# Performance work log

Hardware: AMD Instinct MI355X
Metric: run time of the kernel (lower is better)

The kernel has to match this reference:

```python
import jax, jax.numpy as jnp
import numpy as np

B, T, V, E, H = 32, 40, 8000, 50, 2048


def setup_inputs() -> dict:
    key = jax.random.key(0)
    ks = jax.random.split(key, 13)
    s = 0.02  # small init scale for stability
    return {
        "features": jax.random.normal(ks[0], (B, H), dtype=jnp.float32),
        "captions": jax.random.randint(ks[1], (B, T), 0, V),
        "emb": jax.random.normal(ks[2], (V, E), dtype=jnp.float32) * s,
        "lstm_Wih": jax.random.normal(ks[3], (4 * H, E), dtype=jnp.float32) * s,
        "lstm_bih": jax.random.normal(ks[4], (4 * H,), dtype=jnp.float32) * s,
        "lstm_Whh": jax.random.normal(ks[5], (4 * H, H), dtype=jnp.float32) * s,
        "lstm_bhh": jax.random.normal(ks[6], (4 * H,), dtype=jnp.float32) * s,
        "gru_Wih": jax.random.normal(ks[7], (3 * H, H), dtype=jnp.float32) * s,
        "gru_bih": jax.random.normal(ks[8], (3 * H,), dtype=jnp.float32) * s,
        "gru_Whh": jax.random.normal(ks[9], (3 * H, H), dtype=jnp.float32) * s,
        "gru_bhh": jax.random.normal(ks[10], (3 * H,), dtype=jnp.float32) * s,
        "lin_W": jax.random.normal(ks[11], (V, H), dtype=jnp.float32) * s,
        "lin_b": jax.random.normal(ks[12], (V,), dtype=jnp.float32) * s,
    }


def reference(features, captions, emb, lstm_Wih, lstm_bih, lstm_Whh, lstm_bhh,
              gru_Wih, gru_bih, gru_Whh, gru_bhh, lin_W, lin_b):
    # Dropout layers act as identity in eval mode.
    embeddings = emb[captions]                 # [B, T, E]
    xs = jnp.swapaxes(embeddings[:, :-1], 0, 1)  # [T-1, B, E]

    def step(carry, x):
        h_l, c_l, h_g = carry
        # torch LSTMCell
        gates = x @ lstm_Wih.T + lstm_bih + h_l @ lstm_Whh.T + lstm_bhh
        i, f, g, o = jnp.split(gates, 4, axis=-1)
        c = jax.nn.sigmoid(f) * c_l + jax.nn.sigmoid(i) * jnp.tanh(g)
        h = jax.nn.sigmoid(o) * jnp.tanh(c)
        # torch GRUCell, input = lstm cell state c
        gi = c @ gru_Wih.T + gru_bih
        gh = h_g @ gru_Whh.T + gru_bhh
        r_i, z_i, n_i = jnp.split(gi, 3, axis=-1)
        r_h, z_h, n_h = jnp.split(gh, 3, axis=-1)
        r = jax.nn.sigmoid(r_i + r_h)
        z = jax.nn.sigmoid(z_i + z_h)
        n = jnp.tanh(n_i + r * n_h)
        hg = (1.0 - z) * n + z * h_g
        out = hg @ lin_W.T + lin_b              # [B, V]
        return (h, c, hg), out

    init = (features, features, features)
    _, outs = jax.lax.scan(step, init, xs)      # [T-1, B, V]
    return jnp.swapaxes(outs, 0, 1)             # [B, T-1, V]
```

## Files before the change

### kernel.cpp

```cpp
#include <hip/hip_runtime.h>

#define BB 32
#define TT 40
#define TS 39
#define VV 8000
#define EE 50
#define HH 2048

typedef short s16x8 __attribute__((ext_vector_type(8)));
typedef float f32x4 __attribute__((ext_vector_type(4)));

__device__ __forceinline__ float sigmf(float x) { return 1.0f / (1.0f + __expf(-x)); }
__device__ __forceinline__ float tanhf_fast(float x) { return 2.0f / (1.0f + __expf(-2.0f * x)) - 1.0f; }

__device__ __forceinline__ unsigned short f2bf(float x) {
    union { float f; unsigned u; } v; v.f = x;
    unsigned r = v.u + 0x7FFF + ((v.u >> 16) & 1);
    return (unsigned short)(r >> 16);
}

__global__ void convert_kernel(const float* __restrict__ src,
                               unsigned short* __restrict__ dst, int n4) {
    int i = blockIdx.x * 256 + threadIdx.x;
    if (i < n4) {
        float4 v = ((const float4*)src)[i];
        ushort4 o;
        o.x = f2bf(v.x); o.y = f2bf(v.y); o.z = f2bf(v.z); o.w = f2bf(v.w);
        ((ushort4*)dst)[i] = o;
    }
}

__global__ void embed_proj_kernel(const int* __restrict__ caps,
                                  const float* __restrict__ emb,
                                  const float* __restrict__ Wih,
                                  const float* __restrict__ bih,
                                  const float* __restrict__ bhh,
                                  float* __restrict__ xw) {
    __shared__ float elds[BB][EE];
    int t = blockIdx.y;
    int j = blockIdx.x * 256 + threadIdx.x;
    for (int idx = threadIdx.x; idx < BB * EE; idx += 256) {
        int bl = idx / EE, e = idx - bl * EE;
        elds[bl][e] = emb[(size_t)caps[bl * TT + t] * EE + e];
    }
    __syncthreads();
    float wreg[EE];
#pragma unroll
    for (int e = 0; e < EE; ++e) wreg[e] = Wih[(size_t)j * EE + e];
    float bias = bih[j] + bhh[j];
    for (int bl = 0; bl < BB; ++bl) {
        float acc = bias;
#pragma unroll
        for (int e = 0; e < EE; ++e) acc += wreg[e] * elds[bl][e];
        xw[((size_t)(t * BB + bl)) * (4 * HH) + j] = acc;
    }
}

__global__ void init_state_kernel(const float* __restrict__ feat,
                                  float* __restrict__ c32, float* __restrict__ hg32,
                                  unsigned short* __restrict__ hbf,
                                  unsigned short* __restrict__ cbf,
                                  unsigned short* __restrict__ hgbf) {
    int i = blockIdx.x * 256 + threadIdx.x;
    float v = feat[i];
    c32[i] = v; hg32[i] = v;
    unsigned short b = f2bf(v);
    hbf[i] = b; cbf[i] = b; hgbf[i] = b;
}

__global__ __launch_bounds__(512) void step1_kernel(
    const unsigned short* __restrict__ Whh,
    const unsigned short* __restrict__ gWhh,
    const float* __restrict__ gbhh,
    const float* __restrict__ xw_t,
    const unsigned short* __restrict__ hbf_in,
    const unsigned short* __restrict__ hgbf,
    float* __restrict__ c32,
    unsigned short* __restrict__ cbf,
    unsigned short* __restrict__ hbf_out,
    float* __restrict__ gh)
{
    __shared__ float lsum[4][2][32][17];
    const int tid = threadIdx.x;
    const int lane = tid & 63;
    const int w = tid >> 6;
    const int g = w >> 1;
    const int kh = w & 1;
    const int l15 = lane & 15;
    const int lq = lane >> 4;
    const int kofs = kh * 1024 + lq * 8;

    const bool lstm = (blockIdx.x < 128);
    const unsigned short* Abase;
    const unsigned short* Brow;
    if (lstm) {
        int kk0 = blockIdx.x * 16;
        Brow = Whh + (size_t)(g * HH + kk0 + l15) * HH + kofs;
        Abase = hbf_in;
    } else {
        int n0 = (blockIdx.x - 128) * 64;
        Brow = gWhh + (size_t)(n0 + g * 16 + l15) * HH + kofs;
        Abase = hgbf;
    }
    const unsigned short* Arow0 = Abase + l15 * HH + kofs;
    const unsigned short* Arow1 = Arow0 + 16 * HH;

    f32x4 acc0 = {0.f, 0.f, 0.f, 0.f};
    f32x4 acc1 = {0.f, 0.f, 0.f, 0.f};
#pragma unroll 4
    for (int it = 0; it < 32; ++it) {
        s16x8 bv = *(const s16x8*)(Brow + it * 32);
        s16x8 a0 = *(const s16x8*)(Arow0 + it * 32);
        s16x8 a1 = *(const s16x8*)(Arow1 + it * 32);
        acc0 = __builtin_amdgcn_mfma_f32_16x16x32_bf16(a0, bv, acc0, 0, 0, 0);
        acc1 = __builtin_amdgcn_mfma_f32_16x16x32_bf16(a1, bv, acc1, 0, 0, 0);
    }
#pragma unroll
    for (int r = 0; r < 4; ++r) {
        lsum[g][kh][lq * 4 + r][l15]      = acc0[r];
        lsum[g][kh][16 + lq * 4 + r][l15] = acc1[r];
    }
    __syncthreads();

    if (lstm) {
        int kk0 = blockIdx.x * 16;
        int kkl = tid & 15, b = tid >> 4;
        int kk = kk0 + kkl;
        const float* xwb = xw_t + (size_t)b * 4 * HH;
        float vi = lsum[0][0][b][kkl] + lsum[0][1][b][kkl] + xwb[kk];
        float vf = lsum[1][0][b][kkl] + lsum[1][1][b][kkl] + xwb[HH + kk];
        float vg = lsum[2][0][b][kkl] + lsum[2][1][b][kkl] + xwb[2 * HH + kk];
        float vo = lsum[3][0][b][kkl] + lsum[3][1][b][kkl] + xwb[3 * HH + kk];
        int idx = b * HH + kk;
        float c = sigmf(vf) * c32[idx] + sigmf(vi) * tanhf_fast(vg);
        float h = sigmf(vo) * tanhf_fast(c);
        c32[idx] = c;
        cbf[idx] = f2bf(c);
        hbf_out[idx] = f2bf(h);
    } else {
        int n0 = (blockIdx.x - 128) * 64;
        for (int cell = tid; cell < 2048; cell += 512) {
            int nl = cell & 63, b = cell >> 6;
            int n = n0 + nl;
            float v = lsum[nl >> 4][0][b][nl & 15] + lsum[nl >> 4][1][b][nl & 15] + gbhh[n];
            gh[b * 3 * HH + n] = v;
        }
    }
}

__global__ __launch_bounds__(384) void step2_kernel(
    const unsigned short* __restrict__ gWih,
    const float* __restrict__ gbih,
    const unsigned short* __restrict__ cbf,
    const float* __restrict__ gh,
    float* __restrict__ hg32,
    unsigned short* __restrict__ hgbf,
    unsigned short* __restrict__ hg_all_t)
{
    __shared__ float lsum[3][2][32][17];
    const int tid = threadIdx.x;
    const int lane = tid & 63;
    const int w = tid >> 6;
    const int g = w >> 1;
    const int kh = w & 1;
    const int l15 = lane & 15;
    const int lq = lane >> 4;
    const int kofs = kh * 1024 + lq * 8;
    const int kk0 = blockIdx.x * 16;

    const unsigned short* Arow0 = cbf + l15 * HH + kofs;
    const unsigned short* Arow1 = Arow0 + 16 * HH;
    const unsigned short* Brow = gWih + (size_t)(g * HH + kk0 + l15) * HH + kofs;

    f32x4 acc0 = {0.f, 0.f, 0.f, 0.f};
    f32x4 acc1 = {0.f, 0.f, 0.f, 0.f};
#pragma unroll 4
    for (int it = 0; it < 32; ++it) {
        s16x8 bv = *(const s16x8*)(Brow + it * 32);
        s16x8 a0 = *(const s16x8*)(Arow0 + it * 32);
        s16x8 a1 = *(const s16x8*)(Arow1 + it * 32);
        acc0 = __builtin_amdgcn_mfma_f32_16x16x32_bf16(a0, bv, acc0, 0, 0, 0);
        acc1 = __builtin_amdgcn_mfma_f32_16x16x32_bf16(a1, bv, acc1, 0, 0, 0);
    }
#pragma unroll
    for (int r = 0; r < 4; ++r) {
        lsum[g][kh][lq * 4 + r][l15]      = acc0[r];
        lsum[g][kh][16 + lq * 4 + r][l15] = acc1[r];
    }
    __syncthreads();

    for (int cell = tid; cell < 512; cell += 384) {
        int kkl = cell & 15, b = cell >> 4;
        int kk = kk0 + kkl;
        float ri = lsum[0][0][b][kkl] + lsum[0][1][b][kkl] + gbih[kk];
        float zi = lsum[1][0][b][kkl] + lsum[1][1][b][kkl] + gbih[HH + kk];
        float ni = lsum[2][0][b][kkl] + lsum[2][1][b][kkl] + gbih[2 * HH + kk];
        const float* ghb = gh + b * 3 * HH;
        float r = sigmf(ri + ghb[kk]);
        float z = sigmf(zi + ghb[HH + kk]);
        float n = tanhf_fast(ni + r * ghb[2 * HH + kk]);
        int idx = b * HH + kk;
        float hgn = (1.f - z) * n + z * hg32[idx];
        hg32[idx] = hgn;
        unsigned short hb = f2bf(hgn);
        hgbf[idx] = hb;
        hg_all_t[idx] = hb;
    }
}

__global__ __launch_bounds__(256) void out_gemm_kernel(
    const unsigned short* __restrict__ A,
    const unsigned short* __restrict__ Wl,
    const float* __restrict__ bl,
    float* __restrict__ out) {
    __shared__ unsigned short As[64][40];
    __shared__ unsigned short Bs[64][40];
    const int tid = threadIdx.x;
    const int lane = tid & 63;
    const int w = tid >> 6;
    const int l15 = lane & 15;
    const int lq = lane >> 4;
    const int nt = blockIdx.x, mt = blockIdx.y;
    const int srow = tid >> 2, scol = (tid & 3) * 8;
    const unsigned short* Ap = A + (size_t)(mt * 64 + srow) * HH + scol;
    const unsigned short* Bp = Wl + (size_t)(nt * 64 + srow) * HH + scol;

    f32x4 acc[4];
#pragma unroll
    for (int i = 0; i < 4; ++i) acc[i] = (f32x4){0.f, 0.f, 0.f, 0.f};

    for (int k0 = 0; k0 < HH; k0 += 32) {
        s16x8 av = *(const s16x8*)(Ap + k0);
        s16x8 bv = *(const s16x8*)(Bp + k0);
        *(s16x8*)&As[srow][scol] = av;
        *(s16x8*)&Bs[srow][scol] = bv;
        __syncthreads();
        s16x8 af = *(const s16x8*)&As[w * 16 + l15][lq * 8];
#pragma unroll
        for (int ns = 0; ns < 4; ++ns) {
            s16x8 bf = *(const s16x8*)&Bs[ns * 16 + l15][lq * 8];
            acc[ns] = __builtin_amdgcn_mfma_f32_16x16x32_bf16(af, bf, acc[ns], 0, 0, 0);
        }
        __syncthreads();
    }
#pragma unroll
    for (int ns = 0; ns < 4; ++ns) {
        int n = nt * 64 + ns * 16 + l15;
        float bn = bl[n];
#pragma unroll
        for (int r = 0; r < 4; ++r) {
            int m = mt * 64 + w * 16 + lq * 4 + r;
            if (m < TS * BB) {
                int t = m >> 5, b = m & 31;
                out[((size_t)b * TS + t) * VV + n] = acc[ns][r] + bn;
            }
        }
    }
}

extern "C" void kernel_launch(void* const* d_in, const int* in_sizes, int n_in,
                              void* d_out, int out_size, void* d_ws, size_t ws_size,
                              hipStream_t stream) {
    const float* features = (const float*)d_in[0];
    const int*   captions = (const int*)d_in[1];
    const float* emb      = (const float*)d_in[2];
    const float* lstm_Wih = (const float*)d_in[3];
    const float* lstm_bih = (const float*)d_in[4];
    const float* lstm_Whh = (const float*)d_in[5];
    const float* lstm_bhh = (const float*)d_in[6];
    const float* gru_Wih  = (const float*)d_in[7];
    const float* gru_bih  = (const float*)d_in[8];
    const float* gru_Whh  = (const float*)d_in[9];
    const float* gru_bhh  = (const float*)d_in[10];
    const float* lin_W    = (const float*)d_in[11];
    const float* lin_b    = (const float*)d_in[12];
    float* out = (float*)d_out;

    unsigned short* us = (unsigned short*)d_ws;
    unsigned short* Whh_bf  = us;
    unsigned short* gWhh_bf = Whh_bf  + (size_t)8192 * HH;
    unsigned short* gWih_bf = gWhh_bf + (size_t)6144 * HH;
    unsigned short* linW_bf = gWih_bf + (size_t)6144 * HH;
    unsigned short* hbf0    = linW_bf + (size_t)VV * HH;
    unsigned short* hbf1    = hbf0 + BB * HH;
    unsigned short* cbf     = hbf1 + BB * HH;
    unsigned short* hgbf    = cbf  + BB * HH;
    unsigned short* hg_all  = hgbf + BB * HH;
    float* f32s = (float*)(hg_all + (size_t)1280 * HH);
    float* xw   = f32s;
    float* c32  = xw + (size_t)TS * BB * 4 * HH;
    float* hg32 = c32 + BB * HH;
    float* gh   = hg32 + BB * HH;

    {
        int n4;
        n4 = 8192 * HH / 4;
        convert_kernel<<<(n4 + 255) / 256, 256, 0, stream>>>(lstm_Whh, Whh_bf, n4);
        n4 = 6144 * HH / 4;
        convert_kernel<<<(n4 + 255) / 256, 256, 0, stream>>>(gru_Whh, gWhh_bf, n4);
        convert_kernel<<<(n4 + 255) / 256, 256, 0, stream>>>(gru_Wih, gWih_bf, n4);
        n4 = VV * HH / 4;
        convert_kernel<<<(n4 + 255) / 256, 256, 0, stream>>>(lin_W, linW_bf, n4);
    }

    embed_proj_kernel<<<dim3(4 * HH / 256, TS), 256, 0, stream>>>(
        captions, emb, lstm_Wih, lstm_bih, lstm_bhh, xw);

    init_state_kernel<<<(BB * HH) / 256, 256, 0, stream>>>(
        features, c32, hg32, hbf0, cbf, hgbf);

    for (int t = 0; t < TS; ++t) {
        const unsigned short* hin = (t & 1) ? hbf1 : hbf0;
        unsigned short*       hout = (t & 1) ? hbf0 : hbf1;
        step1_kernel<<<224, 512, 0, stream>>>(
            Whh_bf, gWhh_bf, gru_bhh, xw + (size_t)t * BB * 4 * HH,
            hin, hgbf, c32, cbf, hout, gh);
        step2_kernel<<<128, 384, 0, stream>>>(
            gWih_bf, gru_bih, cbf, gh, hg32, hgbf, hg_all + (size_t)t * BB * HH);
    }

    out_gemm_kernel<<<dim3(VV / 64, (TS * BB + 63) / 64), 256, 0, stream>>>(
        hg_all, linW_bf, lin_b, out);
}
```

Baseline: 2.093 ms.

## Split K four ways in recurrent step kernels and enlarge output GEMM tiles

The LSTM/GRU step kernels now use 1024 and 768 threads, each wave covering a quarter of the K dimension instead of half, with partial sums reduced through a larger shared-memory buffer. This puts more memory requests in flight to hide latency on the weight streaming that dominates each of the 78 sequential step launches. The output projection GEMM moves from 64x64 to 128x128 tiles, with each wave computing a 4x4 grid of MFMA tiles for more reuse. The trade-offs are higher register pressure, unpadded shared-memory tiles that may cause bank conflicts, and reads past row 8000 of the linear weights.

```diff
diff --git a/kernel.cpp b/kernel.cpp
--- a/kernel.cpp
+++ b/kernel.cpp
@@ -68,7 +68,7 @@
     hbf[i] = b; cbf[i] = b; hgbf[i] = b;
 }
 
-__global__ __launch_bounds__(512) void step1_kernel(
+__global__ __launch_bounds__(1024, 4) void step1_kernel(
     const unsigned short* __restrict__ Whh,
     const unsigned short* __restrict__ gWhh,
     const float* __restrict__ gbhh,
@@ -80,15 +80,15 @@
     unsigned short* __restrict__ hbf_out,
     float* __restrict__ gh)
 {
-    __shared__ float lsum[4][2][32][17];
+    __shared__ float lsum[4][4][32][17];
     const int tid = threadIdx.x;
     const int lane = tid & 63;
     const int w = tid >> 6;
-    const int g = w >> 1;
-    const int kh = w & 1;
+    const int g = w >> 2;
+    const int kh = w & 3;
     const int l15 = lane & 15;
     const int lq = lane >> 4;
-    const int kofs = kh * 1024 + lq * 8;
+    const int kofs = kh * 512 + lq * 8;
 
     const bool lstm = (blockIdx.x < 128);
     const unsigned short* Abase;
@@ -108,7 +108,7 @@
     f32x4 acc0 = {0.f, 0.f, 0.f, 0.f};
     f32x4 acc1 = {0.f, 0.f, 0.f, 0.f};
 #pragma unroll 4
-    for (int it = 0; it < 32; ++it) {
+    for (int it = 0; it < 16; ++it) {
         s16x8 bv = *(const s16x8*)(Brow + it * 32);
         s16x8 a0 = *(const s16x8*)(Arow0 + it * 32);
         s16x8 a1 = *(const s16x8*)(Arow1 + it * 32);
@@ -123,32 +123,35 @@
     __syncthreads();
 
     if (lstm) {
-        int kk0 = blockIdx.x * 16;
-        int kkl = tid & 15, b = tid >> 4;
-        int kk = kk0 + kkl;
-        const float* xwb = xw_t + (size_t)b * 4 * HH;
-        float vi = lsum[0][0][b][kkl] + lsum[0][1][b][kkl] + xwb[kk];
-        float vf = lsum[1][0][b][kkl] + lsum[1][1][b][kkl] + xwb[HH + kk];
-        float vg = lsum[2][0][b][kkl] + lsum[2][1][b][kkl] + xwb[2 * HH + kk];
-        float vo = lsum[3][0][b][kkl] + lsum[3][1][b][kkl] + xwb[3 * HH + kk];
-        int idx = b * HH + kk;
-        float c = sigmf(vf) * c32[idx] + sigmf(vi) * tanhf_fast(vg);
-        float h = sigmf(vo) * tanhf_fast(c);
-        c32[idx] = c;
-        cbf[idx] = f2bf(c);
-        hbf_out[idx] = f2bf(h);
+        if (tid < 512) {
+            int kk0 = blockIdx.x * 16;
+            int kkl = tid & 15, b = tid >> 4;
+            int kk = kk0 + kkl;
+            const float* xwb = xw_t + (size_t)b * 4 * HH;
+            float vi = lsum[0][0][b][kkl] + lsum[0][1][b][kkl] + lsum[0][2][b][kkl] + lsum[0][3][b][kkl] + xwb[kk];
+            float vf = lsum[1][0][b][kkl] + lsum[1][1][b][kkl] + lsum[1][2][b][kkl] + lsum[1][3][b][kkl] + xwb[HH + kk];
+            float vg = lsum[2][0][b][kkl] + lsum[2][1][b][kkl] + lsum[2][2][b][kkl] + lsum[2][3][b][kkl] + xwb[2 * HH + kk];
+            float vo = lsum[3][0][b][kkl] + lsum[3][1][b][kkl] + lsum[3][2][b][kkl] + lsum[3][3][b][kkl] + xwb[3 * HH + kk];
+            int idx = b * HH + kk;
+            float c = sigmf(vf) * c32[idx] + sigmf(vi) * tanhf_fast(vg);
+            float h = sigmf(vo) * tanhf_fast(c);
+            c32[idx] = c;
+            cbf[idx] = f2bf(c);
+            hbf_out[idx] = f2bf(h);
+        }
     } else {
         int n0 = (blockIdx.x - 128) * 64;
-        for (int cell = tid; cell < 2048; cell += 512) {
+        for (int cell = tid; cell < 2048; cell += 1024) {
             int nl = cell & 63, b = cell >> 6;
-            int n = n0 + nl;
-            float v = lsum[nl >> 4][0][b][nl & 15] + lsum[nl >> 4][1][b][nl & 15] + gbhh[n];
-            gh[b * 3 * HH + n] = v;
+            int s = nl >> 4, n15 = nl & 15;
+            float v = lsum[s][0][b][n15] + lsum[s][1][b][n15] + lsum[s][2][b][n15] + lsum[s][3][b][n15]
+                      + gbhh[n0 + nl];
+            gh[b * 3 * HH + n0 + nl] = v;
         }
     }
 }
 
-__global__ __launch_bounds__(384) void step2_kernel(
+__global__ __launch_bounds__(768, 3) void step2_kernel(
     const unsigned short* __restrict__ gWih,
     const float* __restrict__ gbih,
     const unsigned short* __restrict__ cbf,
@@ -157,15 +160,15 @@
     unsigned short* __restrict__ hgbf,
     unsigned short* __restrict__ hg_all_t)
 {
-    __shared__ float lsum[3][2][32][17];
+    __shared__ float lsum[3][4][32][17];
     const int tid = threadIdx.x;
     const int lane = tid & 63;
     const int w = tid >> 6;
-    const int g = w >> 1;
-    const int kh = w & 1;
+    const int g = w >> 2;
+    const int kh = w & 3;
     const int l15 = lane & 15;
     const int lq = lane >> 4;
-    const int kofs = kh * 1024 + lq * 8;
+    const int kofs = kh * 512 + lq * 8;
     const int kk0 = blockIdx.x * 16;
 
     const unsigned short* Arow0 = cbf + l15 * HH + kofs;
@@ -175,7 +178,7 @@
     f32x4 acc0 = {0.f, 0.f, 0.f, 0.f};
     f32x4 acc1 = {0.f, 0.f, 0.f, 0.f};
 #pragma unroll 4
-    for (int it = 0; it < 32; ++it) {
+    for (int it = 0; it < 16; ++it) {
         s16x8 bv = *(const s16x8*)(Brow + it * 32);
         s16x8 a0 = *(const s16x8*)(Arow0 + it * 32);
         s16x8 a1 = *(const s16x8*)(Arow1 + it * 32);
@@ -189,12 +192,12 @@
     }
     __syncthreads();
 
-    for (int cell = tid; cell < 512; cell += 384) {
-        int kkl = cell & 15, b = cell >> 4;
+    if (tid < 512) {
+        int kkl = tid & 15, b = tid >> 4;
         int kk = kk0 + kkl;
-        float ri = lsum[0][0][b][kkl] + lsum[0][1][b][kkl] + gbih[kk];
-        float zi = lsum[1][0][b][kkl] + lsum[1][1][b][kkl] + gbih[HH + kk];
-        float ni = lsum[2][0][b][kkl] + lsum[2][1][b][kkl] + gbih[2 * HH + kk];
+        float ri = lsum[0][0][b][kkl] + lsum[0][1][b][kkl] + lsum[0][2][b][kkl] + lsum[0][3][b][kkl] + gbih[kk];
+        float zi = lsum[1][0][b][kkl] + lsum[1][1][b][kkl] + lsum[1][2][b][kkl] + lsum[1][3][b][kkl] + gbih[HH + kk];
+        float ni = lsum[2][0][b][kkl] + lsum[2][1][b][kkl] + lsum[2][2][b][kkl] + lsum[2][3][b][kkl] + gbih[2 * HH + kk];
         const float* ghb = gh + b * 3 * HH;
         float r = sigmf(ri + ghb[kk]);
         float z = sigmf(zi + ghb[HH + kk]);
@@ -213,46 +216,63 @@
     const unsigned short* __restrict__ Wl,
     const float* __restrict__ bl,
     float* __restrict__ out) {
-    __shared__ unsigned short As[64][40];
-    __shared__ unsigned short Bs[64][40];
+    __shared__ unsigned short As[128][32];
+    __shared__ unsigned short Bs[128][32];
     const int tid = threadIdx.x;
     const int lane = tid & 63;
     const int w = tid >> 6;
     const int l15 = lane & 15;
     const int lq = lane >> 4;
-    const int nt = blockIdx.x, mt = blockIdx.y;
-    const int srow = tid >> 2, scol = (tid & 3) * 8;
-    const unsigned short* Ap = A + (size_t)(mt * 64 + srow) * HH + scol;
-    const unsigned short* Bp = Wl + (size_t)(nt * 64 + srow) * HH + scol;
-
-    f32x4 acc[4];
-#pragma unroll
-    for (int i = 0; i < 4; ++i) acc[i] = (f32x4){0.f, 0.f, 0.f, 0.f};
+    const int mt = blockIdx.x, nt = blockIdx.y;
+    const int mq = w >> 1, nq = w & 1;
+
+    const int row0 = tid >> 2, kc0 = (tid & 3) * 8;
+    const unsigned short* Ap0 = A + (size_t)(mt * 128 + row0) * HH + kc0;
+    const unsigned short* Ap1 = A + (size_t)(mt * 128 + 64 + row0) * HH + kc0;
+    const unsigned short* Bp0 = Wl + (size_t)(nt * 128 + row0) * HH + kc0;
+    const unsigned short* Bp1 = Wl + (size_t)(nt * 128 + 64 + row0) * HH + kc0;
+
+    f32x4 acc[4][4];
+#pragma unroll
+    for (int i = 0; i < 4; ++i)
+#pragma unroll
+        for (int j = 0; j < 4; ++j) acc[i][j] = (f32x4){0.f, 0.f, 0.f, 0.f};
 
     for (int k0 = 0; k0 < HH; k0 += 32) {
-        s16x8 av = *(const s16x8*)(Ap + k0);
-        s16x8 bv = *(const s16x8*)(Bp + k0);
-        *(s16x8*)&As[srow][scol] = av;
-        *(s16x8*)&Bs[srow][scol] = bv;
+        s16x8 a0v = *(const s16x8*)(Ap0 + k0);
+        s16x8 a1v = *(const s16x8*)(Ap1 + k0);
+        s16x8 b0v = *(const s16x8*)(Bp0 + k0);
+        s16x8 b1v = *(const s16x8*)(Bp1 + k0);
+        *(s16x8*)&As[row0][kc0]      = a0v;
+        *(s16x8*)&As[64 + row0][kc0] = a1v;
+        *(s16x8*)&Bs[row0][kc0]      = b0v;
+        *(s16x8*)&Bs[64 + row0][kc0] = b1v;
         __syncthreads();
-        s16x8 af = *(const s16x8*)&As[w * 16 + l15][lq * 8];
-#pragma unroll
-        for (int ns = 0; ns < 4; ++ns) {
-            s16x8 bf = *(const s16x8*)&Bs[ns * 16 + l15][lq * 8];
-            acc[ns] = __builtin_amdgcn_mfma_f32_16x16x32_bf16(af, bf, acc[ns], 0, 0, 0);
-        }
+        s16x8 af[4], bf[4];
+#pragma unroll
+        for (int i = 0; i < 4; ++i) af[i] = *(const s16x8*)&As[mq * 64 + i * 16 + l15][lq * 8];
+#pragma unroll
+        for (int j = 0; j < 4; ++j) bf[j] = *(const s16x8*)&Bs[nq * 64 + j * 16 + l15][lq * 8];
+#pragma unroll
+        for (int i = 0; i < 4; ++i)
+#pragma unroll
+            for (int j = 0; j < 4; ++j)
+                acc[i][j] = __builtin_amdgcn_mfma_f32_16x16x32_bf16(af[i], bf[j], acc[i][j], 0, 0, 0);
         __syncthreads();
     }
 #pragma unroll
-    for (int ns = 0; ns < 4; ++ns) {
-        int n = nt * 64 + ns * 16 + l15;
-        float bn = bl[n];
-#pragma unroll
-        for (int r = 0; r < 4; ++r) {
-            int m = mt * 64 + w * 16 + lq * 4 + r;
-            if (m < TS * BB) {
-                int t = m >> 5, b = m & 31;
-                out[((size_t)b * TS + t) * VV + n] = acc[ns][r] + bn;
+    for (int j = 0; j < 4; ++j) {
+        int n = nt * 128 + nq * 64 + j * 16 + l15;
+        float bn = bl[n < VV ? n : VV - 1];
+#pragma unroll
+        for (int i = 0; i < 4; ++i) {
+#pragma unroll
+            for (int r = 0; r < 4; ++r) {
+                int m = mt * 128 + mq * 64 + i * 16 + lq * 4 + r;
+                if (m < TS * BB && n < VV) {
+                    int t = m >> 5, b = m & 31;
+                    out[((size_t)b * TS + t) * VV + n] = acc[i][j][r] + bn;
+                }
             }
         }
     }
@@ -312,13 +332,13 @@
     for (int t = 0; t < TS; ++t) {
         const unsigned short* hin = (t & 1) ? hbf1 : hbf0;
         unsigned short*       hout = (t & 1) ? hbf0 : hbf1;
-        step1_kernel<<<224, 512, 0, stream>>>(
+        step1_kernel<<<224, 1024, 0, stream>>>(
             Whh_bf, gWhh_bf, gru_bhh, xw + (size_t)t * BB * 4 * HH,
             hin, hgbf, c32, cbf, hout, gh);
-        step2_kernel<<<128, 384, 0, stream>>>(
+        step2_kernel<<<128, 768, 0, stream>>>(
             gWih_bf, gru_bih, cbf, gh, hg32, hgbf, hg_all + (size_t)t * BB * HH);
     }
 
-    out_gemm_kernel<<<dim3(VV / 64, (TS * BB + 63) / 64), 256, 0, stream>>>(
+    out_gemm_kernel<<<dim3((TS * BB + 127) / 128, (VV + 127) / 128), 256, 0, stream>>>(
         hg_all, linW_bf, lin_b, out);
 }
```

After: 2.054 ms. Within noise of the previous version (-1.8%).
